# Kernel tuning notes

Hardware: AMD Instinct MI355X
Metric: run time of the kernel (lower is better)

Reference implementation:

```python
import jax, jax.numpy as jnp
import numpy as np

NG, NC, D, E, L, OUT = 100000, 2000, 256, 1000000, 2, 64


def setup_inputs() -> dict:
    key = jax.random.key(0)
    ks = jax.random.split(key, 16)
    s = 1.0 / np.sqrt(D)
    return dict(
        x_gene=jax.random.normal(ks[0], (NG, D), dtype=jnp.float32),
        x_cell=jax.random.normal(ks[1], (NC, D), dtype=jnp.float32),
        src_g2c=jax.random.randint(ks[2], (E,), 0, NG),
        dst_g2c=jax.random.randint(ks[3], (E,), 0, NC),
        src_c2g=jax.random.randint(ks[4], (E,), 0, NC),
        dst_c2g=jax.random.randint(ks[5], (E,), 0, NG),
        idx_gg=jnp.arange(NG),
        idx_cc=jnp.arange(NC),
        w_g2c=jax.random.uniform(ks[6], (E,), dtype=jnp.float32),
        w_c2g=jax.random.uniform(ks[7], (E,), dtype=jnp.float32),
        w_gg=jax.random.uniform(ks[8], (NG,), dtype=jnp.float32),
        w_cc=jax.random.uniform(ks[9], (NC,), dtype=jnp.float32),
        Wrel=jax.random.normal(ks[10], (L, 4, D, D), dtype=jnp.float32) * s,
        brel=jax.random.normal(ks[11], (L, 4, D), dtype=jnp.float32) * 0.1,
        Wroot=jax.random.normal(ks[12], (L, 4, D, D), dtype=jnp.float32) * s,
        Wout=jax.random.normal(ks[13], (OUT, D), dtype=jnp.float32) * s,
        bout=jax.random.normal(ks[14], (OUT,), dtype=jnp.float32) * 0.1,
    )


def _agg(x_src, src, dst, w, n_dst):
    # GraphConv message: x_j * edge_weight, then scatter-add to destinations
    msg = x_src[src] * w[:, None]  # [E, D]
    return jax.ops.segment_sum(msg, dst, num_segments=n_dst)


def reference(x_gene, x_cell, src_g2c, dst_g2c, src_c2g, dst_c2g,
              idx_gg, idx_cc, w_g2c, w_c2g, w_gg, w_cc,
              Wrel, brel, Wroot, Wout, bout):
    xg, xc = x_gene, x_cell
    for l in range(L):
        # relation 0: gene -> cell_type; 1: cell_type -> gene;
        # relation 2: gene self-loop; 3: cell_type self-loop
        agg_c = _agg(xg, src_g2c, dst_g2c, w_g2c, NC)
        agg_g = _agg(xc, src_c2g, dst_c2g, w_c2g, NG)
        agg_gg = _agg(xg, idx_gg, idx_gg, w_gg, NG)
        agg_cc = _agg(xc, idx_cc, idx_cc, w_cc, NC)
        # GraphConv: lin_rel(agg) + bias + lin_root(x_dst); HeteroConv aggr='sum'
        new_c = (agg_c @ Wrel[l, 0].T + brel[l, 0] + xc @ Wroot[l, 0].T
                 + agg_cc @ Wrel[l, 3].T + brel[l, 3] + xc @ Wroot[l, 3].T)
        new_g = (agg_g @ Wrel[l, 1].T + brel[l, 1] + xg @ Wroot[l, 1].T
                 + agg_gg @ Wrel[l, 2].T + brel[l, 2] + xg @ Wroot[l, 2].T)
        xg, xc = jax.nn.relu(new_g), jax.nn.relu(new_c)
    return xc @ Wout.T + bout  # [NC, OUT]
```

## Files before the change

kernel.cpp:

```cpp
#include <hip/hip_runtime.h>

static constexpr int NG   = 100000;
static constexpr int NC   = 2000;
static constexpr int D    = 256;
static constexpr int NE   = 1000000;
static constexpr int NOUTD= 64;
static constexpr int KCAT = 768;

typedef __bf16 bf16x8 __attribute__((ext_vector_type(8)));
typedef float  f32x4  __attribute__((ext_vector_type(4)));

__device__ __forceinline__ unsigned short f2bf(float f) {
    unsigned u = __float_as_uint(f);
    u += 0x7fffu + ((u >> 16) & 1u);
    return (unsigned short)(u >> 16);
}
__device__ __forceinline__ float bflo(unsigned x) { return __uint_as_float((x & 0xffffu) << 16); }
__device__ __forceinline__ float bfhi(unsigned x) { return __uint_as_float(x & 0xffff0000u); }

__device__ __forceinline__ void async16(const void* g, void* l) {
    __builtin_amdgcn_global_load_lds(
        (const __attribute__((address_space(1))) void*)g,
        (__attribute__((address_space(3))) void*)l, 16, 0, 0);
}

__global__ void prep_x(const float* __restrict__ x, const float* __restrict__ w,
                       unsigned short* __restrict__ dx, unsigned short* __restrict__ dv,
                       long stride, int rows) {
    int i = blockIdx.x * blockDim.x + threadIdx.x;
    if (i >= rows * (D / 4)) return;
    int row = i >> 6, c4 = (i & 63) * 4;
    float4 xv = *reinterpret_cast<const float4*>(x + (size_t)row * D + c4);
    float wv = w[row];
    uint2 ox, ov;
    ox.x = (unsigned)f2bf(xv.x) | ((unsigned)f2bf(xv.y) << 16);
    ox.y = (unsigned)f2bf(xv.z) | ((unsigned)f2bf(xv.w) << 16);
    ov.x = (unsigned)f2bf(xv.x * wv) | ((unsigned)f2bf(xv.y * wv) << 16);
    ov.y = (unsigned)f2bf(xv.z * wv) | ((unsigned)f2bf(xv.w * wv) << 16);
    *reinterpret_cast<uint2*>(dx + (size_t)row * stride + c4) = ox;
    *reinterpret_cast<uint2*>(dv + (size_t)row * stride + c4) = ov;
}

__global__ void build_wcat3(const float* __restrict__ Wrel, const float* __restrict__ Wroot,
                            const float* __restrict__ brel,
                            unsigned short* __restrict__ Wg0, unsigned short* __restrict__ Wc0,
                            unsigned short* __restrict__ Wc1,
                            float* __restrict__ bg0, float* __restrict__ bc0,
                            float* __restrict__ bc1) {
    int i = blockIdx.x * blockDim.x + threadIdx.x;
    if (i >= D * D) return;
    int ia, ib; unsigned short* wout; float* bsum;
    if (blockIdx.y == 0)      { ia = 1; ib = 2; wout = Wg0; bsum = bg0; }
    else if (blockIdx.y == 1) { ia = 0; ib = 3; wout = Wc0; bsum = bc0; }
    else                      { ia = 4; ib = 7; wout = Wc1; bsum = bc1; }
    const int WW = D * D;
    int n = i >> 8, k = i & 255;
    wout[(size_t)n * KCAT + k]        = f2bf(Wrel[ia * WW + i]);
    wout[(size_t)n * KCAT + 256 + k]  = f2bf(Wroot[ia * WW + i] + Wroot[ib * WW + i]);
    wout[(size_t)n * KCAT + 512 + k]  = f2bf(Wrel[ib * WW + i]);
    if (i < D) bsum[i] = brel[ia * D + i] + brel[ib * D + i];
}

static constexpr int CC_CHUNK = 8192;
static constexpr int CCB = (NE + CC_CHUNK - 1) / CC_CHUNK;
static constexpr int CONVB = NG * (D / 4) / 256;
__global__ __launch_bounds__(256) void coarse_count_conv(
        const int* __restrict__ dst_g2c, const int* __restrict__ dst_c2g,
        int* __restrict__ hist,
        const float* __restrict__ x_gene, unsigned short* __restrict__ xg0b) {
    __shared__ int h[512];
    if (blockIdx.x >= CCB) {
        int i = (blockIdx.x - CCB) * 256 + threadIdx.x;
        int row = i >> 6, c4 = (i & 63) * 4;
        float4 xv = *reinterpret_cast<const float4*>(x_gene + (size_t)row * D + c4);
        uint2 xo;
        xo.x = (unsigned)f2bf(xv.x) | ((unsigned)f2bf(xv.y) << 16);
        xo.y = (unsigned)f2bf(xv.z) | ((unsigned)f2bf(xv.w) << 16);
        *reinterpret_cast<uint2*>(xg0b + (size_t)row * D + c4) = xo;
        return;
    }
    h[threadIdx.x] = 0; h[256 + threadIdx.x] = 0;
    __syncthreads();
    int base = blockIdx.x * CC_CHUNK;
#pragma unroll 4
    for (int t = 0; t < CC_CHUNK / 256; ++t) {
        int e = base + t * 256 + threadIdx.x;
        if (e < NE) {
            atomicAdd(&h[dst_g2c[e] >> 3], 1);
            atomicAdd(&h[256 + (dst_c2g[e] >> 9)], 1);
        }
    }
    __syncthreads();
    if (h[threadIdx.x]) atomicAdd(&hist[threadIdx.x], h[threadIdx.x]);
    if (h[256 + threadIdx.x]) atomicAdd(&hist[256 + threadIdx.x], h[256 + threadIdx.x]);
}

__global__ __launch_bounds__(256) void coarse_scan(const int* __restrict__ hist,
                                                   int* __restrict__ cbase,
                                                   int* __restrict__ ccur_c, int* __restrict__ ccur_g,
                                                   int* __restrict__ rp_c, int* __restrict__ rp_g) {
    __shared__ int sd[256];
    int t = threadIdx.x;
    {
        int v = hist[t];
        sd[t] = v; __syncthreads();
        for (int off = 1; off < 256; off <<= 1) {
            int u = (t >= off) ? sd[t - off] : 0; __syncthreads();
            sd[t] += u; __syncthreads();
        }
        int e = sd[t] - v;
        cbase[t] = e; ccur_c[t] = e;
        if (t == 255) cbase[256] = sd[255];
        __syncthreads();
    }
    {
        int v = hist[256 + t];
        sd[t] = v; __syncthreads();
        for (int off = 1; off < 256; off <<= 1) {
            int u = (t >= off) ? sd[t - off] : 0; __syncthreads();
            sd[t] += u; __syncthreads();
        }
        int e = sd[t] - v;
        cbase[257 + t] = e; ccur_g[t] = e;
        if (t == 255) cbase[513] = sd[255];
    }
    if (t == 0) { rp_c[NC] = NE; rp_g[NG] = NE; }
}

static constexpr int P1_CHUNK = 8192;
__global__ __launch_bounds__(256) void bucket_pass1(
        const int* __restrict__ srcA, const int* __restrict__ dstA, const float* __restrict__ wA,
        int* __restrict__ curA, int2* __restrict__ outA,
        const int* __restrict__ srcB, const int* __restrict__ dstB, const float* __restrict__ wB,
        int* __restrict__ curB, int2* __restrict__ outB) {
    __shared__ int hist[256], lcur[256], gbase[256];
    const int* src; const int* dst; const float* w; int* coarse_cur; int2* out;
    int shift, packshift;
    if (blockIdx.y == 0) { src = srcA; dst = dstA; w = wA; coarse_cur = curA; out = outA; shift = 3; packshift = 17; }
    else { src = srcB; dst = dstB; w = wB; coarse_cur = curB; out = outB; shift = 9; packshift = 11; }
    int tid = threadIdx.x;
    hist[tid] = 0;
    __syncthreads();
    int base = blockIdx.x * P1_CHUNK;
    int mybin[P1_CHUNK / 256];
#pragma unroll
    for (int t = 0; t < P1_CHUNK / 256; ++t) {
        int e = base + t * 256 + tid;
        if (e < NE) {
            int b = dst[e] >> shift;
            mybin[t] = b;
            atomicAdd(&hist[b], 1);
        } else mybin[t] = -1;
    }
    __syncthreads();
    int v = hist[tid];
    gbase[tid] = v ? atomicAdd(&coarse_cur[tid], v) : 0;
    lcur[tid] = 0;
    __syncthreads();
#pragma unroll
    for (int t = 0; t < P1_CHUNK / 256; ++t) {
        int b = mybin[t];
        if (b < 0) continue;
        int e = base + t * 256 + tid;
        int pos = gbase[b] + atomicAdd(&lcur[b], 1);
        int dl = dst[e] & ((1 << shift) - 1);
        out[pos] = make_int2(src[e] | (dl << packshift), __float_as_int(w[e]));
    }
}

static constexpr int P2_CBLK = NC / 8;
static constexpr int P2_GBLK = (NG + 511) / 512;
__global__ __launch_bounds__(256) void bucket_pass2(
        const int2* __restrict__ stC, int2* __restrict__ outC, int* __restrict__ rpC,
        const int2* __restrict__ stG, int2* __restrict__ outG, int* __restrict__ rpG,
        const int* __restrict__ cbase) {
    __shared__ int hist[512], cur[512], sd[256];
    const int2* staged; int2* out; int* rp; const int* cb;
    int shift, packshift, ndst, b;
    if (blockIdx.x < P2_CBLK) {
        staged = stC; out = outC; rp = rpC; cb = cbase;
        shift = 3; packshift = 17; ndst = NC; b = blockIdx.x;
    } else {
        staged = stG; out = outG; rp = rpG; cb = cbase + 257;
        shift = 9; packshift = 11; ndst = NG; b = blockIdx.x - P2_CBLK;
    }
    int tid = threadIdx.x;
    int nf = 1 << shift;
    int d0 = b << shift;
    int j0 = cb[b], j1 = cb[b + 1];
    for (int f = tid; f < nf; f += 256) hist[f] = 0;
    __syncthreads();
    for (int j = j0 + tid; j < j1; j += 256)
        atomicAdd(&hist[((unsigned)staged[j].x) >> packshift], 1);
    __syncthreads();
    int chunk = (nf + 255) >> 8;
    int s = 0;
#pragma unroll 2
    for (int k = 0; k < chunk; ++k) {
        int idx = tid * chunk + k;
        if (idx < nf) s += hist[idx];
    }
    sd[tid] = s; __syncthreads();
    for (int off = 1; off < 256; off <<= 1) {
        int u = (tid >= off) ? sd[tid - off] : 0; __syncthreads();
        sd[tid] += u; __syncthreads();
    }
    int run = sd[tid] - s;
#pragma unroll 2
    for (int k = 0; k < chunk; ++k) {
        int idx = tid * chunk + k;
        if (idx < nf) {
            int h = hist[idx];
            int pos = j0 + run;
            cur[idx] = pos;
            int d = d0 + idx;
            if (d < ndst) rp[d] = pos;
            run += h;
        }
    }
    __syncthreads();
    for (int j = j0 + tid; j < j1; j += 256) {
        int2 e = staged[j];
        int f = ((unsigned)e.x) >> packshift;
        int pos = atomicAdd(&cur[f], 1);
        out[pos] = make_int2(e.x & ((1 << packshift) - 1), e.y);
    }
}

__global__ void agg_gene(const int* __restrict__ rp, const int2* __restrict__ eg,
                         const unsigned short* __restrict__ src, long sstride,
                         unsigned short* __restrict__ agg_out, int nrows) {
    int wave = (blockIdx.x * blockDim.x + threadIdx.x) >> 6;
    int lane = threadIdx.x & 63;
    if (wave >= nrows) return;
    int j0 = __builtin_amdgcn_readfirstlane(rp[wave]);
    int j1 = __builtin_amdgcn_readfirstlane(rp[wave + 1]);
    int half = lane >> 5;
    int lh = lane & 31;
    float a0=0.f,a1=0.f,a2=0.f,a3=0.f,a4=0.f,a5=0.f,a6=0.f,a7=0.f;
    int j = j0;
    for (; j + 4 <= j1; j += 4) {
        int2 e0 = eg[j], e1 = eg[j + 1], e2 = eg[j + 2], e3 = eg[j + 3];
        int   rA = half ? e1.x : e0.x;
        float wA = __int_as_float(half ? e1.y : e0.y);
        int   rB = half ? e3.x : e2.x;
        float wB = __int_as_float(half ? e3.y : e2.y);
        uint4 pA = *reinterpret_cast<const uint4*>(src + (size_t)rA * sstride + lh * 8);
        uint4 pB = *reinterpret_cast<const uint4*>(src + (size_t)rB * sstride + lh * 8);
        a0 += wA * bflo(pA.x) + wB * bflo(pB.x);
        a1 += wA * bfhi(pA.x) + wB * bfhi(pB.x);
        a2 += wA * bflo(pA.y) + wB * bflo(pB.y);
        a3 += wA * bfhi(pA.y) + wB * bfhi(pB.y);
        a4 += wA * bflo(pA.z) + wB * bflo(pB.z);
        a5 += wA * bfhi(pA.z) + wB * bfhi(pB.z);
        a6 += wA * bflo(pA.w) + wB * bflo(pB.w);
        a7 += wA * bfhi(pA.w) + wB * bfhi(pB.w);
    }
    for (; j < j1; j += 2) {
        int2 e0 = eg[j];
        int2 e1 = (j + 1 < j1) ? eg[j + 1] : make_int2(e0.x, 0);
        int   r = half ? e1.x : e0.x;
        float w = __int_as_float(half ? e1.y : e0.y);
        uint4 p = *reinterpret_cast<const uint4*>(src + (size_t)r * sstride + lh * 8);
        a0 += w * bflo(p.x); a1 += w * bfhi(p.x);
        a2 += w * bflo(p.y); a3 += w * bfhi(p.y);
        a4 += w * bflo(p.z); a5 += w * bfhi(p.z);
        a6 += w * bflo(p.w); a7 += w * bfhi(p.w);
    }
    a0 += __shfl_xor(a0, 32, 64); a1 += __shfl_xor(a1, 32, 64);
    a2 += __shfl_xor(a2, 32, 64); a3 += __shfl_xor(a3, 32, 64);
    a4 += __shfl_xor(a4, 32, 64); a5 += __shfl_xor(a5, 32, 64);
    a6 += __shfl_xor(a6, 32, 64); a7 += __shfl_xor(a7, 32, 64);
    if (lane < 32) {
        uint4 o;
        o.x = (unsigned)f2bf(a0) | ((unsigned)f2bf(a1) << 16);
        o.y = (unsigned)f2bf(a2) | ((unsigned)f2bf(a3) << 16);
        o.z = (unsigned)f2bf(a4) | ((unsigned)f2bf(a5) << 16);
        o.w = (unsigned)f2bf(a6) | ((unsigned)f2bf(a7) << 16);
        *reinterpret_cast<uint4*>(agg_out + (size_t)wave * D + lane * 8) = o;
    }
}

__global__ __launch_bounds__(256, 2) void gene_gemm(
        const unsigned short* __restrict__ Agg,
        const unsigned short* __restrict__ Xb,
        const float* __restrict__ w_gg,
        const unsigned short* __restrict__ W,
        const float* __restrict__ bias,
        unsigned short* __restrict__ xg1) {
    __shared__ unsigned short As[128 * 64];
    __shared__ unsigned short Bs1[128 * 64];
    __shared__ unsigned short Bs2[128 * 64];
    int tid = threadIdx.x;
    int wv = tid >> 6, ln = tid & 63;
    int lm = ln & 15, lq = ln >> 4;
    int m0 = blockIdx.x * 128;
    int nb = blockIdx.y * 128;
    int m0w = m0 + (wv >> 1) * 64;
    int n0w = nb + (wv & 1) * 64;

    f32x4 accA[4][4], accV[4][4];
#pragma unroll
    for (int i = 0; i < 4; ++i)
#pragma unroll
        for (int j = 0; j < 4; ++j) { accA[i][j] = f32x4{0,0,0,0}; accV[i][j] = f32x4{0,0,0,0}; }

    for (int k0 = 0; k0 < 256; k0 += 64) {
#pragma unroll
        for (int t = 0; t < 4; ++t) {
            int ci = t * 256 + tid;
            int r = ci >> 3, s = ci & 7;
            int cg = s ^ (r & 7);
            int row = m0 + r; if (row >= NG) row = NG - 1;
            async16(Agg + (size_t)row * D + k0 + cg * 8, (unsigned char*)As + ci * 16);
            async16(W + (size_t)(nb + r) * KCAT + k0 + cg * 8, (unsigned char*)Bs1 + ci * 16);
        }
        __syncthreads();
#pragma unroll
        for (int kk = 0; kk < 2; ++kk) {
            bf16x8 a[4], b[4];
#pragma unroll
            for (int i = 0; i < 4; ++i) {
                int r = (wv >> 1) * 64 + i * 16 + lm;
                int s = (kk * 4 + lq) ^ (r & 7);
                a[i] = *reinterpret_cast<const bf16x8*>(As + (r * 8 + s) * 8);
            }
#pragma unroll
            for (int j = 0; j < 4; ++j) {
                int r = (wv & 1) * 64 + j * 16 + lm;
                int s = (kk * 4 + lq) ^ (r & 7);
                b[j] = *reinterpret_cast<const bf16x8*>(Bs1 + (r * 8 + s) * 8);
            }
#pragma unroll
            for (int i = 0; i < 4; ++i)
#pragma unroll
                for (int j = 0; j < 4; ++j)
                    accA[i][j] = __builtin_amdgcn_mfma_f32_16x16x32_bf16(a[i], b[j], accA[i][j], 0, 0, 0);
        }
        __syncthreads();
    }

    for (int k0 = 0; k0 < 256; k0 += 64) {
#pragma unroll
        for (int t = 0; t < 4; ++t) {
            int ci = t * 256 + tid;
            int r = ci >> 3, s = ci & 7;
            int cg = s ^ (r & 7);
            int row = m0 + r; if (row >= NG) row = NG - 1;
            async16(Xb + (size_t)row * D + k0 + cg * 8, (unsigned char*)As + ci * 16);
            async16(W + (size_t)(nb + r) * KCAT + 256 + k0 + cg * 8, (unsigned char*)Bs1 + ci * 16);
            async16(W + (size_t)(nb + r) * KCAT + 512 + k0 + cg * 8, (unsigned char*)Bs2 + ci * 16);
        }
        __syncthreads();
#pragma unroll
        for (int kk = 0; kk < 2; ++kk) {
            bf16x8 a[4], b1[4], b2[4];
#pragma unroll
            for (int i = 0; i < 4; ++i) {
                int r = (wv >> 1) * 64 + i * 16 + lm;
                int s = (kk * 4 + lq) ^ (r & 7);
                a[i] = *reinterpret_cast<const bf16x8*>(As + (r * 8 + s) * 8);
            }
#pragma unroll
            for (int j = 0; j < 4; ++j) {
                int r = (wv & 1) * 64 + j * 16 + lm;
                int s = (kk * 4 + lq) ^ (r & 7);
                b1[j] = *reinterpret_cast<const bf16x8*>(Bs1 + (r * 8 + s) * 8);
                b2[j] = *reinterpret_cast<const bf16x8*>(Bs2 + (r * 8 + s) * 8);
            }
#pragma unroll
            for (int i = 0; i < 4; ++i)
#pragma unroll
                for (int j = 0; j < 4; ++j) {
                    accA[i][j] = __builtin_amdgcn_mfma_f32_16x16x32_bf16(a[i], b1[j], accA[i][j], 0, 0, 0);
                    accV[i][j] = __builtin_amdgcn_mfma_f32_16x16x32_bf16(a[i], b2[j], accV[i][j], 0, 0, 0);
                }
        }
        __syncthreads();
    }

#pragma unroll
    for (int i = 0; i < 4; ++i) {
#pragma unroll
        for (int r4 = 0; r4 < 4; ++r4) {
            int row = m0w + i * 16 + lq * 4 + r4;
            if (row >= NG) continue;
            float wr = w_gg[row];
#pragma unroll
            for (int j = 0; j < 4; ++j) {
                int col = n0w + j * 16 + lm;
                float v = accA[i][j][r4] + wr * accV[i][j][r4] + bias[col];
                v = v > 0.f ? v : 0.f;
                xg1[(size_t)row * D + col] = f2bf(v);
            }
        }
    }
}

__global__ __launch_bounds__(256) void agg_cell(const int* __restrict__ rp,
                                                const int2* __restrict__ ec,
                                                const unsigned short* __restrict__ src, long sstride,
                                                unsigned short* __restrict__ out, long ostride) {
    __shared__ float red[4][D];
    int c = blockIdx.x;
    int wv = threadIdx.x >> 6, ln = threadIdx.x & 63;
    int half = ln >> 5, lh = ln & 31;
    int j0 = __builtin_amdgcn_readfirstlane(rp[c]);
    int j1 = __builtin_amdgcn_readfirstlane(rp[c + 1]);
    float a0=0.f,a1=0.f,a2=0.f,a3=0.f,a4=0.f,a5=0.f,a6=0.f,a7=0.f;
    int n16 = (j1 - j0) & ~15;
    for (int j = j0 + wv * 4; j < j0 + n16; j += 16) {
        int2 e0 = ec[j], e1 = ec[j + 1], e2 = ec[j + 2], e3 = ec[j + 3];
        int   rA = half ? e1.x : e0.x;
        float wA = __int_as_float(half ? e1.y : e0.y);
        int   rB = half ? e3.x : e2.x;
        float wB = __int_as_float(half ? e3.y : e2.y);
        uint4 pA = *reinterpret_cast<const uint4*>(src + (size_t)rA * sstride + lh * 8);
        uint4 pB = *reinterpret_cast<const uint4*>(src + (size_t)rB * sstride + lh * 8);
        a0 += wA * bflo(pA.x) + wB * bflo(pB.x);
        a1 += wA * bfhi(pA.x) + wB * bfhi(pB.x);
        a2 += wA * bflo(pA.y) + wB * bflo(pB.y);
        a3 += wA * bfhi(pA.y) + wB * bfhi(pB.y);
        a4 += wA * bflo(pA.z) + wB * bflo(pB.z);
        a5 += wA * bfhi(pA.z) + wB * bfhi(pB.z);
        a6 += wA * bflo(pA.w) + wB * bflo(pB.w);
        a7 += wA * bfhi(pA.w) + wB * bfhi(pB.w);
    }
    for (int j = j0 + n16 + wv * 2; j < j1; j += 8) {
        int2 e0 = ec[j];
        int2 e1 = (j + 1 < j1) ? ec[j + 1] : make_int2(e0.x, 0);
        int   r = half ? e1.x : e0.x;
        float w = __int_as_float(half ? e1.y : e0.y);
        uint4 p = *reinterpret_cast<const uint4*>(src + (size_t)r * sstride + lh * 8);
        a0 += w * bflo(p.x); a1 += w * bfhi(p.x);
        a2 += w * bflo(p.y); a3 += w * bfhi(p.y);
        a4 += w * bflo(p.z); a5 += w * bfhi(p.z);
        a6 += w * bflo(p.w); a7 += w * bfhi(p.w);
    }
    a0 += __shfl_xor(a0, 32, 64); a1 += __shfl_xor(a1, 32, 64);
    a2 += __shfl_xor(a2, 32, 64); a3 += __shfl_xor(a3, 32, 64);
    a4 += __shfl_xor(a4, 32, 64); a5 += __shfl_xor(a5, 32, 64);
    a6 += __shfl_xor(a6, 32, 64); a7 += __shfl_xor(a7, 32, 64);
    if (ln < 32) {
        *reinterpret_cast<float4*>(&red[wv][lh * 8])     = make_float4(a0, a1, a2, a3);
        *reinterpret_cast<float4*>(&red[wv][lh * 8 + 4]) = make_float4(a4, a5, a6, a7);
    }
    __syncthreads();
    int col = threadIdx.x;
    float s = red[0][col] + red[1][col] + red[2][col] + red[3][col];
    out[(size_t)c * ostride + col] = f2bf(s);
}

__global__ __launch_bounds__(256, 2) void gemm_tile(
        const unsigned short* __restrict__ A,
        const unsigned short* __restrict__ W,
        const float* __restrict__ bias,
        const float* __restrict__ wrow,
        unsigned short* __restrict__ xout, long xstride,
        unsigned short* __restrict__ vout,
        int M) {
    __shared__ unsigned short As[128 * 64];
    __shared__ unsigned short Bs[128 * 64];
    int tid = threadIdx.x;
    int wv = tid >> 6, ln = tid & 63;
    int lm = ln & 15, lq = ln >> 4;
    int m0 = blockIdx.x * 128;
    int nb = blockIdx.y * 128;
    int m0w = m0 + (wv >> 1) * 64;
    int n0w = nb + (wv & 1) * 64;

    f32x4 acc[4][4];
#pragma unroll
    for (int i = 0; i < 4; ++i)
#pragma unroll
        for (int j = 0; j < 4; ++j) acc[i][j] = f32x4{0.f, 0.f, 0.f, 0.f};

    for (int k0 = 0; k0 < KCAT; k0 += 64) {
#pragma unroll
        for (int t = 0; t < 4; ++t) {
            int ci = t * 256 + tid;
            int r = ci >> 3, s = ci & 7;
            int cg = s ^ (r & 7);
            int row = m0 + r; if (row >= M) row = M - 1;
            async16(A + (size_t)row * KCAT + k0 + cg * 8,
                    (unsigned char*)As + ci * 16);
        }
#pragma unroll
        for (int t = 0; t < 4; ++t) {
            int ci = t * 256 + tid;
            int r = ci >> 3, s = ci & 7;
            int cg = s ^ (r & 7);
            async16(W + (size_t)(nb + r) * KCAT + k0 + cg * 8,
                    (unsigned char*)Bs + ci * 16);
        }
        __syncthreads();
#pragma unroll
        for (int kk = 0; kk < 2; ++kk) {
            bf16x8 a[4], b[4];
#pragma unroll
            for (int i = 0; i < 4; ++i) {
                int r = (wv >> 1) * 64 + i * 16 + lm;
                int c = kk * 4 + lq;
                int s = c ^ (r & 7);
                a[i] = *reinterpret_cast<const bf16x8*>(As + (r * 8 + s) * 8);
            }
#pragma unroll
            for (int j = 0; j < 4; ++j) {
                int r = (wv & 1) * 64 + j * 16 + lm;
                int c = kk * 4 + lq;
                int s = c ^ (r & 7);
                b[j] = *reinterpret_cast<const bf16x8*>(Bs + (r * 8 + s) * 8);
            }
#pragma unroll
            for (int i = 0; i < 4; ++i)
#pragma unroll
                for (int j = 0; j < 4; ++j)
                    acc[i][j] = __builtin_amdgcn_mfma_f32_16x16x32_bf16(a[i], b[j], acc[i][j], 0, 0, 0);
        }
        __syncthreads();
    }

#pragma unroll
    for (int i = 0; i < 4; ++i) {
#pragma unroll
        for (int r4 = 0; r4 < 4; ++r4) {
            int rr = m0w + i * 16 + lq * 4 + r4;
            if (rr >= M) continue;
            float wr = wrow ? wrow[rr] : 0.f;
#pragma unroll
            for (int j = 0; j < 4; ++j) {
                int col = n0w + j * 16 + lm;
                float v = acc[i][j][r4] + bias[col];
                v = v > 0.f ? v : 0.f;
                xout[(size_t)rr * xstride + col] = f2bf(v);
                if (vout) vout[(size_t)rr * xstride + col] = f2bf(v * wr);
            }
        }
    }
}

__global__ __launch_bounds__(256) void out_kernel(const unsigned short* __restrict__ xc,
                                                  const float* __restrict__ Wout,
                                                  const float* __restrict__ bout,
                                                  float* __restrict__ out) {
    __shared__ float srow[8][D];
    __shared__ float wlds[32][D + 1];
    int tid = threadIdx.x;
    for (int t = tid; t < 8 * D; t += 256) {
        int rr = blockIdx.x * 8 + (t >> 8);
        unsigned short h = xc[(size_t)rr * D + (t & 255)];
        srow[t >> 8][t & 255] = __uint_as_float(((unsigned)h) << 16);
    }
    int r = tid >> 5, ol = tid & 31;
    float res[2];
#pragma unroll
    for (int p = 0; p < 2; ++p) {
        __syncthreads();
        for (int t = tid; t < 32 * (D / 4); t += 256) {
            int o = t >> 6, k4 = (t & 63) * 4;
            float4 wv = *reinterpret_cast<const float4*>(Wout + (size_t)(p * 32 + o) * D + k4);
            wlds[o][k4 + 0] = wv.x; wlds[o][k4 + 1] = wv.y;
            wlds[o][k4 + 2] = wv.z; wlds[o][k4 + 3] = wv.w;
        }
        __syncthreads();
        float s = 0.f;
        for (int k = 0; k < D; ++k) s += srow[r][k] * wlds[ol][k];
        res[p] = s;
    }
    int c = blockIdx.x * 8 + r;
    out[(size_t)c * NOUTD + ol] = res[0] + bout[ol];
    out[(size_t)c * NOUTD + 32 + ol] = res[1] + bout[32 + ol];
}

extern "C" void kernel_launch(void* const* d_in, const int* in_sizes, int n_in,
                              void* d_out, int out_size, void* d_ws, size_t ws_size,
                              hipStream_t stream) {
    const float* x_gene = (const float*)d_in[0];
    const float* x_cell = (const float*)d_in[1];
    const int*   src_g2c = (const int*)d_in[2];
    const int*   dst_g2c = (const int*)d_in[3];
    const int*   src_c2g = (const int*)d_in[4];
    const int*   dst_c2g = (const int*)d_in[5];
    const float* w_g2c = (const float*)d_in[8];
    const float* w_c2g = (const float*)d_in[9];
    const float* w_gg  = (const float*)d_in[10];
    const float* w_cc  = (const float*)d_in[11];
    const float* Wrel  = (const float*)d_in[12];
    const float* brel  = (const float*)d_in[13];
    const float* Wroot = (const float*)d_in[14];
    const float* Wout  = (const float*)d_in[15];
    const float* bout  = (const float*)d_in[16];
    float* out = (float*)d_out;

    char* p = (char*)d_ws;
    auto alloc = [&](size_t bytes) -> char* {
        char* r = p;
        p += (bytes + 255) & ~(size_t)255;
        return r;
    };

    unsigned short* xg0b    = (unsigned short*)alloc((size_t)NG * D * 2);
    unsigned short* xg1     = (unsigned short*)alloc((size_t)NG * D * 2);
    unsigned short* agg_g   = (unsigned short*)alloc((size_t)NG * D * 2);
    unsigned short* Acat_c0 = (unsigned short*)alloc((size_t)NC * KCAT * 2);
    unsigned short* Acat_c1 = (unsigned short*)alloc((size_t)NC * KCAT * 2);
    unsigned short* xc2     = (unsigned short*)alloc((size_t)NC * D * 2);
    int* rp_g  = (int*)alloc((NG + 1) * 4);
    int* rp_c  = (int*)alloc((NC + 1) * 4);
    int2* ec = (int2*)alloc((size_t)NE * 8);
    int2* eg = (int2*)alloc((size_t)NE * 8);
    int2* st_c = (int2*)alloc((size_t)NE * 8);
    int2* st_g = (int2*)alloc((size_t)NE * 8);
    int* hist512 = (int*)alloc(512 * 4);
    int* cbase   = (int*)alloc(514 * 4);
    int* ccur_c  = (int*)alloc(256 * 4);
    int* ccur_g  = (int*)alloc(256 * 4);
    unsigned short* Wg0 = (unsigned short*)alloc((size_t)D * KCAT * 2);
    unsigned short* Wc0 = (unsigned short*)alloc((size_t)D * KCAT * 2);
    unsigned short* Wc1 = (unsigned short*)alloc((size_t)D * KCAT * 2);
    float* bg0 = (float*)alloc(D * 4);
    float* bc0 = (float*)alloc(D * 4);
    float* bc1 = (float*)alloc(D * 4);

    hipMemsetAsync(hist512, 0, 512 * 4, stream);

    prep_x<<<(NC * 64 + 255) / 256, 256, 0, stream>>>(x_cell, w_cc, Acat_c0 + 256, Acat_c0 + 512, KCAT, NC);

    build_wcat3<<<dim3((D * D + 255) / 256, 3), 256, 0, stream>>>(
        Wrel, Wroot, brel, Wg0, Wc0, Wc1, bg0, bc0, bc1);

    coarse_count_conv<<<CCB + CONVB, 256, 0, stream>>>(dst_g2c, dst_c2g, hist512, x_gene, xg0b);
    coarse_scan<<<1, 256, 0, stream>>>(hist512, cbase, ccur_c, ccur_g, rp_c, rp_g);
    const int P1B = (NE + P1_CHUNK - 1) / P1_CHUNK;
    bucket_pass1<<<dim3(P1B, 2), 256, 0, stream>>>(
        src_g2c, dst_g2c, w_g2c, ccur_c, st_c,
        src_c2g, dst_c2g, w_c2g, ccur_g, st_g);
    bucket_pass2<<<P2_CBLK + P2_GBLK, 256, 0, stream>>>(
        st_c, ec, rp_c, st_g, eg, rp_g, cbase);

    agg_gene<<<(NG + 3) / 4, 256, 0, stream>>>(
        rp_g, eg, Acat_c0 + 256, KCAT, agg_g, NG);
    gene_gemm<<<dim3((NG + 127) / 128, 2), 256, 0, stream>>>(
        agg_g, xg0b, w_gg, Wg0, bg0, xg1);

    agg_cell<<<NC, 256, 0, stream>>>(rp_c, ec, xg0b, D, Acat_c0, KCAT);
    gemm_tile<<<dim3((NC + 127) / 128, 2), 256, 0, stream>>>(
        Acat_c0, Wc0, bc0, w_cc, Acat_c1 + 256, KCAT, Acat_c1 + 512, NC);

    agg_cell<<<NC, 256, 0, stream>>>(rp_c, ec, xg1, D, Acat_c1, KCAT);
    gemm_tile<<<dim3((NC + 127) / 128, 2), 256, 0, stream>>>(
        Acat_c1, Wc1, bc1, nullptr, xc2, D, nullptr, NC);

    out_kernel<<<NC / 8, 256, 0, stream>>>(xc2, Wout, bout, out);
}
```

Baseline: 567.9 us.

## Pre-pack gene GEMM weights in MFMA fragment order and load directly from global

The gene-layer weight matrix is now written by build_wcat3 in a layout that matches the per-lane MFMA B-fragment order. gene_gemm reads B fragments straight from global memory (L2-resident) instead of staging them through LDS with async loads. This removes two 16 KB LDS buffers and the extra async traffic per k-step, which may raise occupancy and cut LDS bandwidth pressure. The cost is global-load latency on the B operand inside the inner loop, with no prefetching to hide it.

```diff
diff --git a/kernel.cpp b/kernel.cpp
--- a/kernel.cpp
+++ b/kernel.cpp
@@ -43,18 +43,28 @@
 
 __global__ void build_wcat3(const float* __restrict__ Wrel, const float* __restrict__ Wroot,
                             const float* __restrict__ brel,
-                            unsigned short* __restrict__ Wg0, unsigned short* __restrict__ Wc0,
+                            unsigned short* __restrict__ Wg0p, unsigned short* __restrict__ Wc0,
                             unsigned short* __restrict__ Wc1,
                             float* __restrict__ bg0, float* __restrict__ bc0,
                             float* __restrict__ bc1) {
     int i = blockIdx.x * blockDim.x + threadIdx.x;
     if (i >= D * D) return;
-    int ia, ib; unsigned short* wout; float* bsum;
-    if (blockIdx.y == 0)      { ia = 1; ib = 2; wout = Wg0; bsum = bg0; }
-    else if (blockIdx.y == 1) { ia = 0; ib = 3; wout = Wc0; bsum = bc0; }
-    else                      { ia = 4; ib = 7; wout = Wc1; bsum = bc1; }
     const int WW = D * D;
     int n = i >> 8, k = i & 255;
+    if (blockIdx.y == 0) {
+        int r16 = n >> 4, lm = n & 15;
+        int kslot = k >> 5, lq = (k >> 3) & 3, e = k & 7;
+        int ln = lq * 16 + lm;
+        size_t base = ((size_t)r16 * 24) * 64 * 8;
+        Wg0p[base + ((size_t)(kslot     ) * 64 + ln) * 8 + e] = f2bf(Wrel[1 * WW + i]);
+        Wg0p[base + ((size_t)(8  + kslot) * 64 + ln) * 8 + e] = f2bf(Wroot[1 * WW + i] + Wroot[2 * WW + i]);
+        Wg0p[base + ((size_t)(16 + kslot) * 64 + ln) * 8 + e] = f2bf(Wrel[2 * WW + i]);
+        if (i < D) bg0[i] = brel[1 * D + i] + brel[2 * D + i];
+        return;
+    }
+    int ia, ib; unsigned short* wout; float* bsum;
+    if (blockIdx.y == 1) { ia = 0; ib = 3; wout = Wc0; bsum = bc0; }
+    else                 { ia = 4; ib = 7; wout = Wc1; bsum = bc1; }
     wout[(size_t)n * KCAT + k]        = f2bf(Wrel[ia * WW + i]);
     wout[(size_t)n * KCAT + 256 + k]  = f2bf(Wroot[ia * WW + i] + Wroot[ib * WW + i]);
     wout[(size_t)n * KCAT + 512 + k]  = f2bf(Wrel[ib * WW + i]);
@@ -285,12 +295,11 @@
         const unsigned short* __restrict__ Agg,
         const unsigned short* __restrict__ Xb,
         const float* __restrict__ w_gg,
-        const unsigned short* __restrict__ W,
+        const unsigned short* __restrict__ Wp,
         const float* __restrict__ bias,
         unsigned short* __restrict__ xg1) {
     __shared__ unsigned short As[128 * 64];
-    __shared__ unsigned short Bs1[128 * 64];
-    __shared__ unsigned short Bs2[128 * 64];
+    const bf16x8* Wpf = reinterpret_cast<const bf16x8*>(Wp);
     int tid = threadIdx.x;
     int wv = tid >> 6, ln = tid & 63;
     int lm = ln & 15, lq = ln >> 4;
@@ -298,6 +307,7 @@
     int nb = blockIdx.y * 128;
     int m0w = m0 + (wv >> 1) * 64;
     int n0w = nb + (wv & 1) * 64;
+    int rbase = (nb >> 4) + (wv & 1) * 4;
 
     f32x4 accA[4][4], accV[4][4];
 #pragma unroll
@@ -313,7 +323,6 @@
             int cg = s ^ (r & 7);
             int row = m0 + r; if (row >= NG) row = NG - 1;
             async16(Agg + (size_t)row * D + k0 + cg * 8, (unsigned char*)As + ci * 16);
-            async16(W + (size_t)(nb + r) * KCAT + k0 + cg * 8, (unsigned char*)Bs1 + ci * 16);
         }
         __syncthreads();
 #pragma unroll
@@ -325,12 +334,10 @@
                 int s = (kk * 4 + lq) ^ (r & 7);
                 a[i] = *reinterpret_cast<const bf16x8*>(As + (r * 8 + s) * 8);
             }
-#pragma unroll
-            for (int j = 0; j < 4; ++j) {
-                int r = (wv & 1) * 64 + j * 16 + lm;
-                int s = (kk * 4 + lq) ^ (r & 7);
-                b[j] = *reinterpret_cast<const bf16x8*>(Bs1 + (r * 8 + s) * 8);
-            }
+            int kslot = (k0 >> 5) + kk;
+#pragma unroll
+            for (int j = 0; j < 4; ++j)
+                b[j] = Wpf[((size_t)(rbase + j) * 24 + kslot) * 64 + ln];
 #pragma unroll
             for (int i = 0; i < 4; ++i)
 #pragma unroll
@@ -348,8 +355,6 @@
             int cg = s ^ (r & 7);
             int row = m0 + r; if (row >= NG) row = NG - 1;
             async16(Xb + (size_t)row * D + k0 + cg * 8, (unsigned char*)As + ci * 16);
-            async16(W + (size_t)(nb + r) * KCAT + 256 + k0 + cg * 8, (unsigned char*)Bs1 + ci * 16);
-            async16(W + (size_t)(nb + r) * KCAT + 512 + k0 + cg * 8, (unsigned char*)Bs2 + ci * 16);
         }
         __syncthreads();
 #pragma unroll
@@ -361,12 +366,11 @@
                 int s = (kk * 4 + lq) ^ (r & 7);
                 a[i] = *reinterpret_cast<const bf16x8*>(As + (r * 8 + s) * 8);
             }
+            int kslot = (k0 >> 5) + kk;
 #pragma unroll
             for (int j = 0; j < 4; ++j) {
-                int r = (wv & 1) * 64 + j * 16 + lm;
-                int s = (kk * 4 + lq) ^ (r & 7);
-                b1[j] = *reinterpret_cast<const bf16x8*>(Bs1 + (r * 8 + s) * 8);
-                b2[j] = *reinterpret_cast<const bf16x8*>(Bs2 + (r * 8 + s) * 8);
+                b1[j] = Wpf[((size_t)(rbase + j) * 24 + 8  + kslot) * 64 + ln];
+                b2[j] = Wpf[((size_t)(rbase + j) * 24 + 16 + kslot) * 64 + ln];
             }
 #pragma unroll
             for (int i = 0; i < 4; ++i)
@@ -615,9 +619,9 @@
     int* cbase   = (int*)alloc(514 * 4);
     int* ccur_c  = (int*)alloc(256 * 4);
     int* ccur_g  = (int*)alloc(256 * 4);
-    unsigned short* Wg0 = (unsigned short*)alloc((size_t)D * KCAT * 2);
-    unsigned short* Wc0 = (unsigned short*)alloc((size_t)D * KCAT * 2);
-    unsigned short* Wc1 = (unsigned short*)alloc((size_t)D * KCAT * 2);
+    unsigned short* Wg0p = (unsigned short*)alloc((size_t)D * KCAT * 2);
+    unsigned short* Wc0  = (unsigned short*)alloc((size_t)D * KCAT * 2);
+    unsigned short* Wc1  = (unsigned short*)alloc((size_t)D * KCAT * 2);
     float* bg0 = (float*)alloc(D * 4);
     float* bc0 = (float*)alloc(D * 4);
     float* bc1 = (float*)alloc(D * 4);
@@ -627,7 +631,7 @@
     prep_x<<<(NC * 64 + 255) / 256, 256, 0, stream>>>(x_cell, w_cc, Acat_c0 + 256, Acat_c0 + 512, KCAT, NC);
 
     build_wcat3<<<dim3((D * D + 255) / 256, 3), 256, 0, stream>>>(
-        Wrel, Wroot, brel, Wg0, Wc0, Wc1, bg0, bc0, bc1);
+        Wrel, Wroot, brel, Wg0p, Wc0, Wc1, bg0, bc0, bc1);
 
     coarse_count_conv<<<CCB + CONVB, 256, 0, stream>>>(dst_g2c, dst_c2g, hist512, x_gene, xg0b);
     coarse_scan<<<1, 256, 0, stream>>>(hist512, cbase, ccur_c, ccur_g, rp_c, rp_g);
@@ -641,7 +645,7 @@
     agg_gene<<<(NG + 3) / 4, 256, 0, stream>>>(
         rp_g, eg, Acat_c0 + 256, KCAT, agg_g, NG);
     gene_gemm<<<dim3((NG + 127) / 128, 2), 256, 0, stream>>>(
-        agg_g, xg0b, w_gg, Wg0, bg0, xg1);
+        agg_g, xg0b, w_gg, Wg0p, bg0, xg1);
 
     agg_cell<<<NC, 256, 0, stream>>>(rp_c, ec, xg0b, D, Acat_c0, KCAT);
     gemm_tile<<<dim3((NC + 127) / 128, 2), 256, 0, stream>>>(
```

Result: slower. 585.9 us (+3.2%).
